# Kernel optimization log

Hardware: AMD Instinct MI355X
Metric: run time of the kernel (lower is better)

Reference implementation:

```python
import jax, jax.numpy as jnp
import numpy as np

N_GENOMES = 30000
N_GENES = 240000
N_SAMPLES = 128
N_SEQS = 80000


def setup_inputs() -> dict:
    key = jax.random.key(0)
    k0, k1, k2, k3, k4 = jax.random.split(key, 5)
    A = jax.random.normal(k0, (N_GENOMES, N_SAMPLES), dtype=jnp.float32)  # log-abundance
    B = jax.random.normal(k1, (N_GENOMES, N_SAMPLES), dtype=jnp.float32)  # log-PTR
    pos = jax.random.uniform(k2, (N_GENES,), dtype=jnp.float32)           # dist from ori, in [0,1)
    genome_idx = jnp.sort(jax.random.randint(k3, (N_GENES,), 0, N_GENOMES))  # block one-hot of `members`
    seq_idx = jax.random.randint(k4, (N_GENES,), 0, N_SEQS)               # gene -> md5 sequence map
    return {"A": A, "B": B, "pos": pos, "genome_idx": genome_idx, "seq_idx": seq_idx}


def reference(A, B, pos, genome_idx, seq_idx):
    # G = members @ A + 1 - dists @ B, where members/dists are one-hot per gene row
    # -> gather rows of A and B by genome assignment, scale B row by gene position.
    G = A[genome_idx] + 1.0 - pos[:, None] * B[genome_idx]   # (m, s)
    # gene_to_seq @ exp(G) -> segment sum of exp(G) over gene->sequence assignment
    return jax.ops.segment_sum(jnp.exp(G), seq_idx, num_segments=N_SEQS)  # (k, s)
```

## Files before the change

kernel.cpp:

```cpp
#include <hip/hip_runtime.h>
#include <hip/hip_fp16.h>

#define N_GENOMES 30000
#define N_GENES   240000
#define N_SAMPLES 128
#define N_SEQS    80000
#define CAP       32

#define SCATTER_BLOCKS  ((N_GENES + 255) / 256)
#define COMPRESS_BLOCKS ((N_GENOMES * 32) / 256)

typedef float        f32x4 __attribute__((ext_vector_type(4)));
typedef unsigned int u32x4 __attribute__((ext_vector_type(4)));

__global__ __launch_bounds__(256) void prep_kernel(
    const float* __restrict__ A,
    const float* __restrict__ B,
    const float* __restrict__ pos,
    const int*   __restrict__ genome_idx,
    const int*   __restrict__ seq_idx,
    int*          __restrict__ cnt,
    unsigned int* __restrict__ bucket,
    float4*       __restrict__ AB16)
{
    int b = blockIdx.x;
    if (b < SCATTER_BLOCKS) {
        int gene = b * 256 + threadIdx.x;
        if (gene >= N_GENES) return;
        int   s = seq_idx[gene];
        int   g = genome_idx[gene];
        float p = pos[gene];
        unsigned int q   = (unsigned int)(p * 131072.0f);
        unsigned int rec = (unsigned int)g | (q << 15);
        int slot = atomicAdd(&cnt[s], 1);
        if (slot < CAP) bucket[s * CAP + slot] = rec;
    } else {
        int idx = (b - SCATTER_BLOCKS) * 256 + threadIdx.x;
        f32x4 a  = __builtin_nontemporal_load((const f32x4*)A + idx);
        f32x4 bb = __builtin_nontemporal_load((const f32x4*)B + idx);
        __half2 h[4];
        h[0] = __floats2half2_rn(a.x + 1.0f, a.y + 1.0f);
        h[1] = __floats2half2_rn(a.z + 1.0f, a.w + 1.0f);
        h[2] = __floats2half2_rn(bb.x, bb.y);
        h[3] = __floats2half2_rn(bb.z, bb.w);
        AB16[idx] = *reinterpret_cast<float4*>(h);
    }
}

__global__ __launch_bounds__(256) void accum_kernel(
    const float4*       __restrict__ AB16,
    const int*          __restrict__ cnt,
    const unsigned int* __restrict__ bucket,
    float*              __restrict__ out)
{
    int idx  = blockIdx.x * blockDim.x + threadIdx.x;
    int seq  = idx >> 5;
    int quad = idx & 31;
    if (seq >= N_SEQS) return;

    const u32x4* bk4 = reinterpret_cast<const u32x4*>(bucket + seq * CAP);
    u32x4 r4 = bk4[0];
    int   n  = cnt[seq];
    if (n > CAP) n = CAP;

    float4 acc = make_float4(0.f, 0.f, 0.f, 0.f);

    {
        unsigned int r[4] = { r4.x, r4.y, r4.z, r4.w };
        float4 raw[4];
        #pragma unroll
        for (int j = 0; j < 4; ++j)
            raw[j] = AB16[(r[j] & 0x7fffu) * 32 + quad];
        #pragma unroll
        for (int j = 0; j < 4; ++j) {
            float p = (float)(r[j] >> 15) * (1.0f / 131072.0f);
            const __half2* hp = reinterpret_cast<const __half2*>(&raw[j]);
            float2 a01 = __half22float2(hp[0]);
            float2 a23 = __half22float2(hp[1]);
            float2 b01 = __half22float2(hp[2]);
            float2 b23 = __half22float2(hp[3]);
            if (j < n) {
                acc.x += __expf(a01.x - p * b01.x);
                acc.y += __expf(a01.y - p * b01.y);
                acc.z += __expf(a23.x - p * b23.x);
                acc.w += __expf(a23.y - p * b23.y);
            }
        }
    }

    if (n > 4) {
        for (int i0 = 4; i0 < n; i0 += 4) {
            u32x4 t4 = bk4[i0 >> 2];
            unsigned int r[4] = { t4.x, t4.y, t4.z, t4.w };
            float4 raw[4];
            #pragma unroll
            for (int j = 0; j < 4; ++j)
                raw[j] = AB16[(r[j] & 0x7fffu) * 32 + quad];
            #pragma unroll
            for (int j = 0; j < 4; ++j) {
                float p = (float)(r[j] >> 15) * (1.0f / 131072.0f);
                const __half2* hp = reinterpret_cast<const __half2*>(&raw[j]);
                float2 a01 = __half22float2(hp[0]);
                float2 a23 = __half22float2(hp[1]);
                float2 b01 = __half22float2(hp[2]);
                float2 b23 = __half22float2(hp[3]);
                if (i0 + j < n) {
                    acc.x += __expf(a01.x - p * b01.x);
                    acc.y += __expf(a01.y - p * b01.y);
                    acc.z += __expf(a23.x - p * b23.x);
                    acc.w += __expf(a23.y - p * b23.y);
                }
            }
        }
    }

    f32x4 o = { acc.x, acc.y, acc.z, acc.w };
    __builtin_nontemporal_store(o, (f32x4*)out + seq * 32 + quad);
}

extern "C" void kernel_launch(void* const* d_in, const int* in_sizes, int n_in,
                              void* d_out, int out_size, void* d_ws, size_t ws_size,
                              hipStream_t stream) {
    const float* A    = (const float*)d_in[0];
    const float* B    = (const float*)d_in[1];
    const float* pos  = (const float*)d_in[2];
    const int*   gidx = (const int*)d_in[3];
    const int*   sidx = (const int*)d_in[4];
    float*       out  = (float*)d_out;

    char*         ws     = (char*)d_ws;
    float4*       AB16   = (float4*)ws;
    int*          cnt    = (int*)(ws + (size_t)N_GENOMES * 32 * 16);
    unsigned int* bucket = (unsigned int*)(cnt + N_SEQS);

    hipMemsetAsync(cnt, 0, (size_t)(N_SEQS + N_SEQS * CAP) * sizeof(int), stream);

    prep_kernel<<<SCATTER_BLOCKS + COMPRESS_BLOCKS, 256, 0, stream>>>(
        A, B, pos, gidx, sidx, cnt, bucket, AB16);

    const int total = N_SEQS * 32;
    accum_kernel<<<total / 256, 256, 0, stream>>>(
        AB16, cnt, bucket, out);
}
```

Before: 126.5 us.

## Reorder sequence processing by first-gene bin to improve genome row locality

```diff
diff --git a/kernel.cpp b/kernel.cpp
--- a/kernel.cpp
+++ b/kernel.cpp
@@ -7,8 +7,14 @@
 #define N_SEQS    80000
 #define CAP       32
 
+#define BIN_SHIFT 5
+#define NBIN2     (N_GENES >> BIN_SHIFT)
+#define CAP2      32
+
 #define SCATTER_BLOCKS  ((N_GENES + 255) / 256)
 #define COMPRESS_BLOCKS ((N_GENOMES * 32) / 256)
+#define SLOT_BLOCKS     (NBIN2 * CAP2 * 32 / 256)
+#define EMPTY_BLOCKS    ((N_SEQS + 255) / 256)
 
 typedef float        f32x4 __attribute__((ext_vector_type(4)));
 typedef unsigned int u32x4 __attribute__((ext_vector_type(4)));
@@ -20,7 +26,9 @@
     const int*   __restrict__ genome_idx,
     const int*   __restrict__ seq_idx,
     int*          __restrict__ cnt,
+    int*          __restrict__ bincnt,
     unsigned int* __restrict__ bucket,
+    int*          __restrict__ order2D,
     float4*       __restrict__ AB16)
 {
     int b = blockIdx.x;
@@ -34,6 +42,11 @@
         unsigned int rec = (unsigned int)g | (q << 15);
         int slot = atomicAdd(&cnt[s], 1);
         if (slot < CAP) bucket[s * CAP + slot] = rec;
+        if (slot == 0) {
+            int bin = gene >> BIN_SHIFT;
+            int os  = atomicAdd(&bincnt[bin], 1);
+            order2D[bin * CAP2 + os] = s;
+        }
     } else {
         int idx = (b - SCATTER_BLOCKS) * 256 + threadIdx.x;
         f32x4 a  = __builtin_nontemporal_load((const f32x4*)A + idx);
@@ -50,13 +63,33 @@
 __global__ __launch_bounds__(256) void accum_kernel(
     const float4*       __restrict__ AB16,
     const int*          __restrict__ cnt,
+    const int*          __restrict__ bincnt,
     const unsigned int* __restrict__ bucket,
+    const int*          __restrict__ order2D,
     float*              __restrict__ out)
 {
-    int idx  = blockIdx.x * blockDim.x + threadIdx.x;
-    int seq  = idx >> 5;
+    int b = blockIdx.x;
+    if (b >= SLOT_BLOCKS) {
+        int seq = (b - SLOT_BLOCKS) * 256 + threadIdx.x;
+        if (seq >= N_SEQS) return;
+        if (cnt[seq] != 0) return;
+        f32x4 z = {0.f, 0.f, 0.f, 0.f};
+        f32x4* o = (f32x4*)out + (size_t)seq * 32;
+        #pragma unroll
+        for (int q = 0; q < 32; ++q)
+            __builtin_nontemporal_store(z, o + q);
+        return;
+    }
+
+    int idx  = b * 256 + threadIdx.x;
+    int w    = idx >> 5;
     int quad = idx & 31;
-    if (seq >= N_SEQS) return;
+    int bin  = w >> 5;
+    int slot = w & 31;
+
+    int m = bincnt[bin];
+    if (slot >= m) return;
+    int seq = order2D[bin * CAP2 + slot];
 
     const u32x4* bk4 = reinterpret_cast<const u32x4*>(bucket + seq * CAP);
     u32x4 r4 = bk4[0];
@@ -115,7 +148,7 @@
     }
 
     f32x4 o = { acc.x, acc.y, acc.z, acc.w };
-    __builtin_nontemporal_store(o, (f32x4*)out + seq * 32 + quad);
+    __builtin_nontemporal_store(o, (f32x4*)out + (size_t)seq * 32 + quad);
 }
 
 extern "C" void kernel_launch(void* const* d_in, const int* in_sizes, int n_in,
@@ -128,17 +161,19 @@
     const int*   sidx = (const int*)d_in[4];
     float*       out  = (float*)d_out;
 
-    char*         ws     = (char*)d_ws;
-    float4*       AB16   = (float4*)ws;
-    int*          cnt    = (int*)(ws + (size_t)N_GENOMES * 32 * 16);
-    unsigned int* bucket = (unsigned int*)(cnt + N_SEQS);
+    char*         ws      = (char*)d_ws;
+    float4*       AB16    = (float4*)ws;
+    int*          cnt     = (int*)(ws + (size_t)N_GENOMES * 32 * 16);
+    int*          bincnt  = cnt + N_SEQS;
+    unsigned int* bucket  = (unsigned int*)(bincnt + NBIN2);
+    int*          order2D = (int*)(bucket + (size_t)N_SEQS * CAP);
 
-    hipMemsetAsync(cnt, 0, (size_t)(N_SEQS + N_SEQS * CAP) * sizeof(int), stream);
+    hipMemsetAsync(cnt, 0,
+                   (size_t)(N_SEQS + NBIN2 + N_SEQS * CAP) * sizeof(int), stream);
 
     prep_kernel<<<SCATTER_BLOCKS + COMPRESS_BLOCKS, 256, 0, stream>>>(
-        A, B, pos, gidx, sidx, cnt, bucket, AB16);
+        A, B, pos, gidx, sidx, cnt, bincnt, bucket, order2D, AB16);
 
-    const int total = N_SEQS * 32;
-    accum_kernel<<<total / 256, 256, 0, stream>>>(
-        AB16, cnt, bucket, out);
+    accum_kernel<<<SLOT_BLOCKS + EMPTY_BLOCKS, 256, 0, stream>>>(
+        AB16, cnt, bincnt, bucket, order2D, out);
 }
```

After: 156.6 us. 23.8% more time.
